# Kernel optimization log

Measured on AMD Instinct MI355X. Metric: run time of the kernel, lower is better.

Reference implementation:

```python
import jax, jax.numpy as jnp
import numpy as np

N = 100000      # nodes
E = 800000      # edges (avg degree 8)
D_IN = 128      # in_channels
HEADS = 8
C = 16          # out_channels per head (heads*C = 128 output dim)
NEG_SLOPE = 0.2  # PyG GATConv default leaky_relu slope


def setup_inputs() -> dict:
    key = jax.random.key(0)
    ks = jax.random.split(key, 12)
    s = 1.0 / np.sqrt(D_IN)
    x = jax.random.normal(ks[0], (N, D_IN), jnp.float32)
    ei = jax.random.randint(ks[1], (2, E), 0, N, jnp.int32)
    return {
        "x": x,
        "ei": ei,
        # conv_in GATConv params
        "W_in": jax.random.normal(ks[2], (D_IN, HEADS * C), jnp.float32) * s,
        "a_src_in": jax.random.normal(ks[3], (HEADS, C), jnp.float32) * s,
        "a_dst_in": jax.random.normal(ks[4], (HEADS, C), jnp.float32) * s,
        "b_in": jnp.zeros((HEADS * C,), jnp.float32),
        # conv_out GATConv params (applied to flipped edges)
        "W_out": jax.random.normal(ks[5], (D_IN, HEADS * C), jnp.float32) * s,
        "a_src_out": jax.random.normal(ks[6], (HEADS, C), jnp.float32) * s,
        "a_dst_out": jax.random.normal(ks[7], (HEADS, C), jnp.float32) * s,
        "b_out": jnp.zeros((HEADS * C,), jnp.float32),
    }


def _gat_conv(x, src, dst, W, a_src, a_dst, b):
    # h: [N, H, C] projected node features
    h = (x @ W).reshape(N, HEADS, C)
    # per-node attention logits [N, H]
    alpha_src = jnp.einsum("nhc,hc->nh", h, a_src)
    alpha_dst = jnp.einsum("nhc,hc->nh", h, a_dst)
    # per-edge logits, message flows src -> dst; softmax grouped by dst
    logits = jax.nn.leaky_relu(alpha_src[src] + alpha_dst[dst], NEG_SLOPE)  # [E, H]
    seg_max = jax.ops.segment_max(logits, dst, num_segments=N)              # [N, H]
    ex = jnp.exp(logits - seg_max[dst])
    denom = jax.ops.segment_sum(ex, dst, num_segments=N)                    # [N, H]
    coef = ex / denom[dst]                                                  # [E, H]
    msg = h[src] * coef[:, :, None]                                         # [E, H, C]
    out = jax.ops.segment_sum(msg, dst, num_segments=N)                     # [N, H, C]
    return out.reshape(N, HEADS * C) + b


def reference(x, ei, W_in, a_src_in, a_dst_in, b_in, W_out, a_src_out, a_dst_out, b_out):
    src, dst = ei[0], ei[1]
    # DirSeq: conv_in on (src->dst), conv_out on flipped edges (dst->src)
    x_in = _gat_conv(x, src, dst, W_in, a_src_in, a_dst_in, b_in)
    x_out = _gat_conv(x, dst, src, W_out, a_src_out, a_dst_out, b_out)
    return x_in + x_out
```

## Files before the change

kernel.cpp:

```cpp
#include <hip/hip_runtime.h>

#define N_NODES 100000
#define N_EDGES 800000
#define NEG 0.2f
#define PB_SHIFT 8
#define PB_NODES 256
#define N_PBKT ((N_NODES + PB_NODES - 1) / PB_NODES)
#define CAP 4096
#define TILE_E 4096
#define EPT 16

typedef __attribute__((ext_vector_type(8))) short bf16x8;
typedef __attribute__((ext_vector_type(4))) float f32x4;

__device__ inline unsigned short f2bf(float f) {
    unsigned u = __float_as_uint(f);
    u += 0x7fffu + ((u >> 16) & 1u);
    return (unsigned short)(u >> 16);
}
__device__ inline float bf2f_lo(unsigned u) { return __uint_as_float(u << 16); }
__device__ inline float bf2f_hi(unsigned u) { return __uint_as_float(u & 0xffff0000u); }

__global__ __launch_bounds__(256) void prep_w_kernel(
    const float* __restrict__ W_in, const float* __restrict__ W_out,
    const float* __restrict__ as_in, const float* __restrict__ ad_in,
    const float* __restrict__ as_out, const float* __restrict__ ad_out,
    unsigned short* __restrict__ Wf, int* __restrict__ gcur,
    int* __restrict__ adj_in, int* __restrict__ adj_out)
{
    const int t = blockIdx.x * 256 + threadIdx.x;
    if (t < 2 * N_PBKT) gcur[t] = 0;
    if (t < 8) { adj_in[N_EDGES + t] = 0; adj_out[N_EDGES + t] = 0; }
    if (t >= 2 * 4 * 9 * 64) return;
    const int lane = t & 63;
    const int rest = t >> 6;
    const int ct  = rest % 9;
    const int kb  = (rest / 9) & 3;
    const int dir = rest / 36;
    const float* W  = dir ? W_out  : W_in;
    const float* as = dir ? as_out : as_in;
    const float* ad = dir ? ad_out : ad_in;
    const int m16 = lane & 15, quad = lane >> 4;

    bf16x8 o;
#pragma unroll
    for (int j = 0; j < 8; ++j) {
        const int k = kb * 32 + quad * 8 + j;
        float v;
        if (ct < 8) {
            v = W[k * 128 + ct * 16 + m16];
        } else {
            const float* av = (m16 < 8) ? as : ad;
            const int hh = m16 & 7;
            v = 0.f;
            for (int c = 0; c < 16; ++c)
                v += W[k * 128 + hh * 16 + c] * av[hh * 16 + c];
        }
        o[j] = (short)f2bf(v);
    }
    *(bf16x8*)&Wf[(long long)t * 8] = o;
}

__global__ __launch_bounds__(256) void gemm_kernel(
    const float* __restrict__ x,
    const unsigned short* __restrict__ Wf,
    unsigned short* __restrict__ h_in, unsigned short* __restrict__ h_out,
    float* __restrict__ asrc_in, float* __restrict__ adst_in,
    float* __restrict__ asrc_out, float* __restrict__ adst_out)
{
    const int dir = blockIdx.y;
    unsigned short* h = dir ? h_out : h_in;
    float* asrc = dir ? asrc_out : asrc_in;
    float* adst = dir ? adst_out : adst_in;

    const int tid  = threadIdx.x;
    const int lane = tid & 63;
    const int wave = tid >> 6;
    const int m16  = lane & 15;
    const int quad = lane >> 4;
    const int rbase = blockIdx.x * 128 + wave * 32;

    f32x4 acc[2][8];
    f32x4 acc_a[2];
#pragma unroll
    for (int rt = 0; rt < 2; ++rt) {
        acc_a[rt] = f32x4{0.f, 0.f, 0.f, 0.f};
#pragma unroll
        for (int ct = 0; ct < 8; ++ct)
            acc[rt][ct] = f32x4{0.f, 0.f, 0.f, 0.f};
    }

    const unsigned short* wf = Wf + (long long)dir * 4 * 9 * 64 * 8;

#pragma unroll
    for (int kb = 0; kb < 4; ++kb) {
        const int k0 = kb * 32 + quad * 8;
        bf16x8 a[2];
#pragma unroll
        for (int rt = 0; rt < 2; ++rt) {
            int r = rbase + rt * 16 + m16;
            r = r < N_NODES ? r : N_NODES - 1;
            const float4 v0 = *(const float4*)&x[(long long)r * 128 + k0];
            const float4 v1 = *(const float4*)&x[(long long)r * 128 + k0 + 4];
            a[rt][0] = (short)f2bf(v0.x); a[rt][1] = (short)f2bf(v0.y);
            a[rt][2] = (short)f2bf(v0.z); a[rt][3] = (short)f2bf(v0.w);
            a[rt][4] = (short)f2bf(v1.x); a[rt][5] = (short)f2bf(v1.y);
            a[rt][6] = (short)f2bf(v1.z); a[rt][7] = (short)f2bf(v1.w);
        }
#pragma unroll
        for (int ct = 0; ct < 9; ++ct) {
            const bf16x8 b = *(const bf16x8*)&wf[(long long)((kb * 9 + ct) * 64 + lane) * 8];
            if (ct < 8) {
                acc[0][ct] = __builtin_amdgcn_mfma_f32_16x16x32_bf16(a[0], b, acc[0][ct], 0, 0, 0);
                acc[1][ct] = __builtin_amdgcn_mfma_f32_16x16x32_bf16(a[1], b, acc[1][ct], 0, 0, 0);
            } else {
                acc_a[0] = __builtin_amdgcn_mfma_f32_16x16x32_bf16(a[0], b, acc_a[0], 0, 0, 0);
                acc_a[1] = __builtin_amdgcn_mfma_f32_16x16x32_bf16(a[1], b, acc_a[1], 0, 0, 0);
            }
        }
    }

#pragma unroll
    for (int rt = 0; rt < 2; ++rt) {
#pragma unroll
        for (int r = 0; r < 4; ++r) {
            const int row = rbase + rt * 16 + quad * 4 + r;
            if (row < N_NODES) {
                unsigned short* hp = &h[(long long)row * 128 + m16];
#pragma unroll
                for (int ct = 0; ct < 8; ++ct)
                    hp[ct * 16] = f2bf(acc[rt][ct][r]);
                const float av = acc_a[rt][r];
                if (m16 < 8) asrc[row * 8 + m16] = av;
                else         adst[row * 8 + (m16 - 8)] = av;
            }
        }
    }
}

__global__ __launch_bounds__(256) void partition_kernel(
    const int* __restrict__ ei, int* __restrict__ gcur,
    int* __restrict__ binned0, int* __restrict__ binned1)
{
    __shared__ int hist0[N_PBKT];
    __shared__ int curs0[N_PBKT];
    __shared__ int hist1[N_PBKT];
    __shared__ int curs1[N_PBKT];
    const int tid = threadIdx.x;
    for (int i = tid; i < N_PBKT; i += 256) { hist0[i] = 0; hist1[i] = 0; }
    __syncthreads();

    const int e0 = blockIdx.x * TILE_E;
    int sv[EPT], tv[EPT];
#pragma unroll
    for (int i = 0; i < EPT; ++i) {
        const int e = e0 + i * 256 + tid;
        if (e < N_EDGES) {
            sv[i] = ei[e];
            tv[i] = ei[N_EDGES + e];
            atomicAdd(&hist0[tv[i] >> PB_SHIFT], 1);
            atomicAdd(&hist1[sv[i] >> PB_SHIFT], 1);
        } else {
            sv[i] = -1; tv[i] = 0;
        }
    }
    __syncthreads();
    for (int b = tid; b < N_PBKT; b += 256) {
        int c = hist0[b];
        curs0[b] = c ? atomicAdd(&gcur[b], c) : 0;
        c = hist1[b];
        curs1[b] = c ? atomicAdd(&gcur[N_PBKT + b], c) : 0;
    }
    __syncthreads();
#pragma unroll
    for (int i = 0; i < EPT; ++i) {
        if (sv[i] >= 0) {
            const int b0 = tv[i] >> PB_SHIFT;
            int pos = atomicAdd(&curs0[b0], 1);
            if (pos < CAP)
                binned0[b0 * CAP + pos] = (sv[i] << 8) | (tv[i] & (PB_NODES - 1));
            const int b1 = sv[i] >> PB_SHIFT;
            pos = atomicAdd(&curs1[b1], 1);
            if (pos < CAP)
                binned1[b1 * CAP + pos] = (tv[i] << 8) | (sv[i] & (PB_NODES - 1));
        }
    }
}

__global__ __launch_bounds__(512) void bucket_scan_kernel(
    const int* __restrict__ gcur,
    int* __restrict__ boffs0, int* __restrict__ boffs1,
    int* __restrict__ offs_in, int* __restrict__ offs_out)
{
    const int dir = blockIdx.x;
    const int* c = gcur + dir * N_PBKT;
    int* bo = dir ? boffs1 : boffs0;

    __shared__ int sm[512];
    const int tid = threadIdx.x;
    const int v = (tid < N_PBKT) ? min(c[tid], CAP) : 0;
    sm[tid] = v;
    __syncthreads();
#pragma unroll
    for (int off = 1; off < 512; off <<= 1) {
        int t = (tid >= off) ? sm[tid - off] : 0;
        __syncthreads();
        sm[tid] += t;
        __syncthreads();
    }
    if (tid < N_PBKT) bo[tid] = sm[tid] - v;
    if (tid == 0) (dir ? offs_out : offs_in)[N_NODES] = N_EDGES;
}

__global__ __launch_bounds__(256) void place_kernel(
    const int* __restrict__ binned0, const int* __restrict__ binned1,
    const int* __restrict__ boffs0, const int* __restrict__ boffs1,
    const int* __restrict__ gcur,
    int* __restrict__ adj_in, int* __restrict__ adj_out,
    int* __restrict__ offs_in, int* __restrict__ offs_out)
{
    const int b   = blockIdx.x;
    const int dir = blockIdx.y;
    const int* bp = (dir ? binned1 : binned0) + b * CAP;
    const int beg = (dir ? boffs1 : boffs0)[b];
    const int cntb = min(gcur[dir * N_PBKT + b], CAP);
    int* adj  = dir ? adj_out  : adj_in;
    int* offs = dir ? offs_out : offs_in;

    const int base = b << PB_SHIFT;
    const int tid = threadIdx.x;

    __shared__ int cnt[PB_NODES];
    __shared__ int sc[PB_NODES];
    __shared__ int cur[PB_NODES];

    cnt[tid] = 0;
    __syncthreads();
    for (int p = tid; p < cntb; p += 256)
        atomicAdd(&cnt[bp[p] & (PB_NODES - 1)], 1);
    __syncthreads();
    const int v = cnt[tid];
    sc[tid] = v;
    __syncthreads();
#pragma unroll
    for (int off = 1; off < PB_NODES; off <<= 1) {
        int t = (tid >= off) ? sc[tid - off] : 0;
        __syncthreads();
        sc[tid] += t;
        __syncthreads();
    }
    const int excl = beg + sc[tid] - v;
    cur[tid] = excl;
    const int node = base + tid;
    if (node < N_NODES) offs[node] = excl;
    __syncthreads();
    for (int p = tid; p < cntb; p += 256) {
        const int pk = bp[p];
        adj[atomicAdd(&cur[pk & (PB_NODES - 1)], 1)] = pk >> 8;
    }
}

__global__ __launch_bounds__(256) void gather_kernel(
    const int* __restrict__ offs_in, const int* __restrict__ adj_in,
    const int* __restrict__ offs_out, const int* __restrict__ adj_out,
    const unsigned short* __restrict__ h_in, const unsigned short* __restrict__ h_out,
    const float* __restrict__ asrc_in, const float* __restrict__ adst_in,
    const float* __restrict__ asrc_out, const float* __restrict__ adst_out,
    const float* __restrict__ b_in, const float* __restrict__ b_out,
    float* __restrict__ out)
{
    int n = (blockIdx.x * 256 + threadIdx.x) >> 6;
    if (n >= N_NODES) return;
    n = __builtin_amdgcn_readfirstlane(n);
    const int lane = threadIdx.x & 63;
    const int c0 = lane * 2;
    const int hh = lane >> 3;
    const int g8 = lane & 7;
    const int grpbase = lane & 56;

    float acc0 = b_in[c0] + b_out[c0];
    float acc1 = b_in[c0 + 1] + b_out[c0 + 1];

#define DIR_BLOCK(OFFS, ADJ, HX, ASRC, ADST)                                   \
    {                                                                          \
        const int beg = OFFS[n], end = OFFS[n + 1];                            \
        if (end > beg) {                                                       \
            const float ad = ADST[n * 8 + hh];                                 \
            float num0 = 0.f, num1 = 0.f, den = 0.f;                           \
            for (int p = beg; p < end; p += 8) {                               \
                const int q = p + g8;                                          \
                const int nbv = ADJ[q];                 \
                float l = ASRC[nbv * 8 + hh] + ad;                             \
                l = l > 0.f ? l : NEG * l;                                     \
                float w = __expf(l);                                           \
                w = (q < end) ? w : 0.f;                                       \
                den += w;                                                      \
                _Pragma("unroll")                                              \
                for (int g = 0; g < 8; ++g) {                                  \
                    const int nb = ADJ[p + g];           \
                    const float w_g = __shfl(w, grpbase + g, 64);              \
                    const unsigned hv = *(const unsigned*)&HX[(long long)nb * 128 + c0]; \
                    num0 += w_g * bf2f_lo(hv);                                 \
                    num1 += w_g * bf2f_hi(hv);                                 \
                }                                                              \
            }                                                                  \
            den += __shfl_xor(den, 1, 64);                                     \
            den += __shfl_xor(den, 2, 64);                                     \
            den += __shfl_xor(den, 4, 64);                                     \
            const float rden = 1.f / den;                                      \
            acc0 += num0 * rden;                                               \
            acc1 += num1 * rden;                                               \
        }                                                                      \
    }

    DIR_BLOCK(offs_in, adj_in, h_in, asrc_in, adst_in)
    DIR_BLOCK(offs_out, adj_out, h_out, asrc_out, adst_out)
#undef DIR_BLOCK

    *(float2*)&out[(long long)n * 128 + c0] = float2{acc0, acc1};
}

extern "C" void kernel_launch(void* const* d_in, const int* in_sizes, int n_in,
                              void* d_out, int out_size, void* d_ws, size_t ws_size,
                              hipStream_t stream) {
    const float* x      = (const float*)d_in[0];
    const int*   ei     = (const int*)  d_in[1];
    const float* W_in   = (const float*)d_in[2];
    const float* as_in  = (const float*)d_in[3];
    const float* ad_in  = (const float*)d_in[4];
    const float* b_in   = (const float*)d_in[5];
    const float* W_out  = (const float*)d_in[6];
    const float* as_out = (const float*)d_in[7];
    const float* ad_out = (const float*)d_in[8];
    const float* b_out  = (const float*)d_in[9];
    float* out = (float*)d_out;

    char* ws = (char*)d_ws;
    const long long NH = (long long)N_NODES * 128;
    unsigned short* h_in  = (unsigned short*)ws;    ws += NH * 2;
    unsigned short* h_out = (unsigned short*)ws;    ws += NH * 2;
    unsigned short* Wf    = (unsigned short*)ws;    ws += 2LL * 4 * 9 * 64 * 8 * 2;
    float* asrc_in   = (float*)ws;                  ws += N_NODES * 8 * 4;
    float* adst_in   = (float*)ws;                  ws += N_NODES * 8 * 4;
    float* asrc_out  = (float*)ws;                  ws += N_NODES * 8 * 4;
    float* adst_out  = (float*)ws;                  ws += N_NODES * 8 * 4;
    int* binned0     = (int*)ws;                    ws += (long long)N_PBKT * CAP * 4;
    int* binned1     = (int*)ws;                    ws += (long long)N_PBKT * CAP * 4;
    int* adj_in      = (int*)ws;                    ws += (N_EDGES + 8) * 4;
    int* adj_out     = (int*)ws;                    ws += (N_EDGES + 8) * 4;
    int* offs_in     = (int*)ws;                    ws += (N_NODES + 1) * 4;
    int* offs_out    = (int*)ws;                    ws += (N_NODES + 1) * 4;
    int* gcur        = (int*)ws;                    ws += 2 * N_PBKT * 4;
    int* boffs0      = (int*)ws;                    ws += (N_PBKT + 1) * 4;
    int* boffs1      = (int*)ws;                    ws += (N_PBKT + 1) * 4;

    prep_w_kernel<<<(2 * 4 * 9 * 64 + 255) / 256, 256, 0, stream>>>(
        W_in, W_out, as_in, ad_in, as_out, ad_out, Wf, gcur, adj_in, adj_out);

    dim3 gemm_grid((N_NODES + 127) / 128, 2);
    gemm_kernel<<<gemm_grid, 256, 0, stream>>>(
        x, Wf, h_in, h_out, asrc_in, adst_in, asrc_out, adst_out);

    partition_kernel<<<(N_EDGES + TILE_E - 1) / TILE_E, 256, 0, stream>>>(
        ei, gcur, binned0, binned1);
    bucket_scan_kernel<<<2, 512, 0, stream>>>(
        gcur, boffs0, boffs1, offs_in, offs_out);
    place_kernel<<<dim3(N_PBKT, 2), 256, 0, stream>>>(
        binned0, binned1, boffs0, boffs1, gcur, adj_in, adj_out, offs_in, offs_out);

    gather_kernel<<<(N_NODES * 64 + 255) / 256, 256, 0, stream>>>(
        offs_in, adj_in, offs_out, adj_out, h_in, h_out,
        asrc_in, adst_in, asrc_out, adst_out, b_in, b_out, out);
}
```

Measured before the change: 271.9 us.

## Merge edge partition with GEMM, fold bucket scan into place kernel

The edge-partition blocks are placed in the same launch as the projection GEMM blocks, so the two independent stages share one grid and can overlap on the GPU. The separate bucket-scan kernel is removed: each place block now computes its own starting offset by summing the preceding bucket counts and reducing them in shared memory. The block also stages its bucket slab in shared memory, so the binned entries are read from global memory once instead of twice. In exchange, each place block does redundant prefix work over up to about 390 buckets, and the fused kernel's shared-memory footprint is sized for the partition path even in GEMM blocks, which may lower occupancy.

```diff
diff --git a/kernel.cpp b/kernel.cpp
--- a/kernel.cpp
+++ b/kernel.cpp
@@ -9,6 +9,8 @@
 #define CAP 4096
 #define TILE_E 4096
 #define EPT 16
+#define PART_BLOCKS ((N_EDGES + TILE_E - 1) / TILE_E)
+#define GEMM_BLOCKS ((N_NODES + 127) / 128)
 
 typedef __attribute__((ext_vector_type(8))) short bf16x8;
 typedef __attribute__((ext_vector_type(4))) float f32x4;
@@ -26,11 +28,13 @@
     const float* __restrict__ as_in, const float* __restrict__ ad_in,
     const float* __restrict__ as_out, const float* __restrict__ ad_out,
     unsigned short* __restrict__ Wf, int* __restrict__ gcur,
-    int* __restrict__ adj_in, int* __restrict__ adj_out)
+    int* __restrict__ adj_in, int* __restrict__ adj_out,
+    int* __restrict__ offs_in, int* __restrict__ offs_out)
 {
     const int t = blockIdx.x * 256 + threadIdx.x;
     if (t < 2 * N_PBKT) gcur[t] = 0;
     if (t < 8) { adj_in[N_EDGES + t] = 0; adj_out[N_EDGES + t] = 0; }
+    if (t == 0) { offs_in[N_NODES] = N_EDGES; offs_out[N_NODES] = N_EDGES; }
     if (t >= 2 * 4 * 9 * 64) return;
     const int lane = t & 63;
     const int rest = t >> 6;
@@ -61,24 +65,75 @@
     *(bf16x8*)&Wf[(long long)t * 8] = o;
 }
 
-__global__ __launch_bounds__(256) void gemm_kernel(
+__global__ __launch_bounds__(256) void mega_kernel(
     const float* __restrict__ x,
     const unsigned short* __restrict__ Wf,
     unsigned short* __restrict__ h_in, unsigned short* __restrict__ h_out,
     float* __restrict__ asrc_in, float* __restrict__ adst_in,
-    float* __restrict__ asrc_out, float* __restrict__ adst_out)
+    float* __restrict__ asrc_out, float* __restrict__ adst_out,
+    const int* __restrict__ ei, int* __restrict__ gcur,
+    int* __restrict__ binned0, int* __restrict__ binned1)
 {
-    const int dir = blockIdx.y;
+    const int tid = threadIdx.x;
+
+    if (blockIdx.x < PART_BLOCKS) {
+        __shared__ int hist0[N_PBKT];
+        __shared__ int curs0[N_PBKT];
+        __shared__ int hist1[N_PBKT];
+        __shared__ int curs1[N_PBKT];
+        for (int i = tid; i < N_PBKT; i += 256) { hist0[i] = 0; hist1[i] = 0; }
+        __syncthreads();
+
+        const int e0 = blockIdx.x * TILE_E;
+        int sv[EPT], tv[EPT];
+#pragma unroll
+        for (int i = 0; i < EPT; ++i) {
+            const int e = e0 + i * 256 + tid;
+            if (e < N_EDGES) {
+                sv[i] = ei[e];
+                tv[i] = ei[N_EDGES + e];
+                atomicAdd(&hist0[tv[i] >> PB_SHIFT], 1);
+                atomicAdd(&hist1[sv[i] >> PB_SHIFT], 1);
+            } else {
+                sv[i] = -1; tv[i] = 0;
+            }
+        }
+        __syncthreads();
+        for (int b = tid; b < N_PBKT; b += 256) {
+            int c = hist0[b];
+            curs0[b] = c ? atomicAdd(&gcur[b], c) : 0;
+            c = hist1[b];
+            curs1[b] = c ? atomicAdd(&gcur[N_PBKT + b], c) : 0;
+        }
+        __syncthreads();
+#pragma unroll
+        for (int i = 0; i < EPT; ++i) {
+            if (sv[i] >= 0) {
+                const int b0 = tv[i] >> PB_SHIFT;
+                int pos = atomicAdd(&curs0[b0], 1);
+                if (pos < CAP)
+                    binned0[b0 * CAP + pos] = (sv[i] << 8) | (tv[i] & (PB_NODES - 1));
+                const int b1 = sv[i] >> PB_SHIFT;
+                pos = atomicAdd(&curs1[b1], 1);
+                if (pos < CAP)
+                    binned1[b1 * CAP + pos] = (tv[i] << 8) | (sv[i] & (PB_NODES - 1));
+            }
+        }
+        return;
+    }
+
+    const int gb  = blockIdx.x - PART_BLOCKS;
+    const int dir = gb >= GEMM_BLOCKS;
+    const int bx  = gb - dir * GEMM_BLOCKS;
     unsigned short* h = dir ? h_out : h_in;
     float* asrc = dir ? asrc_out : asrc_in;
     float* adst = dir ? adst_out : adst_in;
 
-    const int tid  = threadIdx.x;
     const int lane = tid & 63;
     const int wave = tid >> 6;
     const int m16  = lane & 15;
     const int quad = lane >> 4;
-    const int rbase = blockIdx.x * 128 + wave * 32;
+    const int rbase = bx * 128 + wave * 32;
 
     f32x4 acc[2][8];
     f32x4 acc_a[2];
@@ -138,83 +193,8 @@
     }
 }
 
-__global__ __launch_bounds__(256) void partition_kernel(
-    const int* __restrict__ ei, int* __restrict__ gcur,
-    int* __restrict__ binned0, int* __restrict__ binned1)
-{
-    __shared__ int hist0[N_PBKT];
-    __shared__ int curs0[N_PBKT];
-    __shared__ int hist1[N_PBKT];
-    __shared__ int curs1[N_PBKT];
-    const int tid = threadIdx.x;
-    for (int i = tid; i < N_PBKT; i += 256) { hist0[i] = 0; hist1[i] = 0; }
-    __syncthreads();
-
-    const int e0 = blockIdx.x * TILE_E;
-    int sv[EPT], tv[EPT];
-#pragma unroll
-    for (int i = 0; i < EPT; ++i) {
-        const int e = e0 + i * 256 + tid;
-        if (e < N_EDGES) {
-            sv[i] = ei[e];
-            tv[i] = ei[N_EDGES + e];
-            atomicAdd(&hist0[tv[i] >> PB_SHIFT], 1);
-            atomicAdd(&hist1[sv[i] >> PB_SHIFT], 1);
-        } else {
-            sv[i] = -1; tv[i] = 0;
-        }
-    }
-    __syncthreads();
-    for (int b = tid; b < N_PBKT; b += 256) {
-        int c = hist0[b];
-        curs0[b] = c ? atomicAdd(&gcur[b], c) : 0;
-        c = hist1[b];
-        curs1[b] = c ? atomicAdd(&gcur[N_PBKT + b], c) : 0;
-    }
-    __syncthreads();
-#pragma unroll
-    for (int i = 0; i < EPT; ++i) {
-        if (sv[i] >= 0) {
-            const int b0 = tv[i] >> PB_SHIFT;
-            int pos = atomicAdd(&curs0[b0], 1);
-            if (pos < CAP)
-                binned0[b0 * CAP + pos] = (sv[i] << 8) | (tv[i] & (PB_NODES - 1));
-            const int b1 = sv[i] >> PB_SHIFT;
-            pos = atomicAdd(&curs1[b1], 1);
-            if (pos < CAP)
-                binned1[b1 * CAP + pos] = (tv[i] << 8) | (sv[i] & (PB_NODES - 1));
-        }
-    }
-}
-
-__global__ __launch_bounds__(512) void bucket_scan_kernel(
-    const int* __restrict__ gcur,
-    int* __restrict__ boffs0, int* __restrict__ boffs1,
-    int* __restrict__ offs_in, int* __restrict__ offs_out)
-{
-    const int dir = blockIdx.x;
-    const int* c = gcur + dir * N_PBKT;
-    int* bo = dir ? boffs1 : boffs0;
-
-    __shared__ int sm[512];
-    const int tid = threadIdx.x;
-    const int v = (tid < N_PBKT) ? min(c[tid], CAP) : 0;
-    sm[tid] = v;
-    __syncthreads();
-#pragma unroll
-    for (int off = 1; off < 512; off <<= 1) {
-        int t = (tid >= off) ? sm[tid - off] : 0;
-        __syncthreads();
-        sm[tid] += t;
-        __syncthreads();
-    }
-    if (tid < N_PBKT) bo[tid] = sm[tid] - v;
-    if (tid == 0) (dir ? offs_out : offs_in)[N_NODES] = N_EDGES;
-}
-
 __global__ __launch_bounds__(256) void place_kernel(
     const int* __restrict__ binned0, const int* __restrict__ binned1,
-    const int* __restrict__ boffs0, const int* __restrict__ boffs1,
     const int* __restrict__ gcur,
     int* __restrict__ adj_in, int* __restrict__ adj_out,
     int* __restrict__ offs_in, int* __restrict__ offs_out)
@@ -222,22 +202,34 @@
     const int b   = blockIdx.x;
     const int dir = blockIdx.y;
     const int* bp = (dir ? binned1 : binned0) + b * CAP;
-    const int beg = (dir ? boffs1 : boffs0)[b];
-    const int cntb = min(gcur[dir * N_PBKT + b], CAP);
+    const int* gc = gcur + dir * N_PBKT;
     int* adj  = dir ? adj_out  : adj_in;
     int* offs = dir ? offs_out : offs_in;
 
     const int base = b << PB_SHIFT;
     const int tid = threadIdx.x;
-
+    const int cntb = min(gc[b], CAP);
+
+    __shared__ int slab[CAP];
     __shared__ int cnt[PB_NODES];
     __shared__ int sc[PB_NODES];
     __shared__ int cur[PB_NODES];
-
+    __shared__ int red[PB_NODES];
+
+    int part = 0;
+    for (int j = tid; j < b; j += 256) part += min(gc[j], CAP);
+    red[tid] = part;
     cnt[tid] = 0;
+    for (int p = tid; p < cntb; p += 256) slab[p] = bp[p];
     __syncthreads();
+#pragma unroll
+    for (int off = 128; off > 0; off >>= 1) {
+        if (tid < off) red[tid] += red[tid + off];
+        __syncthreads();
+    }
+    const int beg = red[0];
     for (int p = tid; p < cntb; p += 256)
-        atomicAdd(&cnt[bp[p] & (PB_NODES - 1)], 1);
+        atomicAdd(&cnt[slab[p] & (PB_NODES - 1)], 1);
     __syncthreads();
     const int v = cnt[tid];
     sc[tid] = v;
@@ -255,7 +247,7 @@
     if (node < N_NODES) offs[node] = excl;
     __syncthreads();
     for (int p = tid; p < cntb; p += 256) {
-        const int pk = bp[p];
+        const int pk = slab[p];
         adj[atomicAdd(&cur[pk & (PB_NODES - 1)], 1)] = pk >> 8;
     }
 }
@@ -351,22 +343,17 @@
     int* offs_in     = (int*)ws;                    ws += (N_NODES + 1) * 4;
     int* offs_out    = (int*)ws;                    ws += (N_NODES + 1) * 4;
     int* gcur        = (int*)ws;                    ws += 2 * N_PBKT * 4;
-    int* boffs0      = (int*)ws;                    ws += (N_PBKT + 1) * 4;
-    int* boffs1      = (int*)ws;                    ws += (N_PBKT + 1) * 4;
 
     prep_w_kernel<<<(2 * 4 * 9 * 64 + 255) / 256, 256, 0, stream>>>(
-        W_in, W_out, as_in, ad_in, as_out, ad_out, Wf, gcur, adj_in, adj_out);
-
-    dim3 gemm_grid((N_NODES + 127) / 128, 2);
-    gemm_kernel<<<gemm_grid, 256, 0, stream>>>(
-        x, Wf, h_in, h_out, asrc_in, adst_in, asrc_out, adst_out);
-
-    partition_kernel<<<(N_EDGES + TILE_E - 1) / TILE_E, 256, 0, stream>>>(
+        W_in, W_out, as_in, ad_in, as_out, ad_out, Wf, gcur,
+        adj_in, adj_out, offs_in, offs_out);
+
+    mega_kernel<<<PART_BLOCKS + 2 * GEMM_BLOCKS, 256, 0, stream>>>(
+        x, Wf, h_in, h_out, asrc_in, adst_in, asrc_out, adst_out,
         ei, gcur, binned0, binned1);
-    bucket_scan_kernel<<<2, 512, 0, stream>>>(
-        gcur, boffs0, boffs1, offs_in, offs_out);
+
     place_kernel<<<dim3(N_PBKT, 2), 256, 0, stream>>>(
-        binned0, binned1, boffs0, boffs1, gcur, adj_in, adj_out, offs_in, offs_out);
+        binned0, binned1, gcur, adj_in, adj_out, offs_in, offs_out);
 
     gather_kernel<<<(N_NODES * 64 + 255) / 256, 256, 0, stream>>>(
         offs_in, adj_in, offs_out, adj_out, h_in, h_out,
```

Measured after the change: 256.0 us (median of 2 runs). 1.06x faster.
